# Optimization experiments

Measured on AMD Instinct MI355X. Metric: run time of the kernel, lower is better.

The kernel has to match this reference:

```python
import jax, jax.numpy as jnp
import numpy as np

# ---- static configuration (matches init_kwargs / input_specs) ----
B, N = 4, 128            # images, proposals per image
C = 256                  # feature channels (in_channels)
HF, WF = 23, 30          # feature map size (input 736x960 / 32)
PH, PW = 7, 7            # pooled_size
SCALE = 1.0 / 32.0       # scale_factor
HIMG, WIMG = HF * 32, WF * 32
KH = HF // PH + 2        # max rows any pooling bin can span
KW = WF // PW + 2        # max cols any pooling bin can span
HID, OUT = 256, 5
NEG = -1e30


def _roi_pool_one(f, box):
    """Quantized ROI max pooling for one proposal.
    f: (C, HF, WF) feature map; box: (4,) [x1,y1,x2,y2] in feature coords.
    Returns (C, PH, PW)."""
    box = jax.lax.stop_gradient(box)  # indices are non-differentiable
    x1 = jnp.clip(jnp.floor(box[0]).astype(jnp.int32), 0, WF - 1)
    y1 = jnp.clip(jnp.floor(box[1]).astype(jnp.int32), 0, HF - 1)
    roi_w = jnp.clip(jnp.ceil(box[2]).astype(jnp.int32) - x1, 1, WF)
    roi_h = jnp.clip(jnp.ceil(box[3]).astype(jnp.int32) - y1, 1, HF)
    ph = jnp.arange(PH)
    pw = jnp.arange(PW)
    hs = y1 + (ph * roi_h) // PH                       # bin row starts (PH,)
    he = y1 + ((ph + 1) * roi_h + PH - 1) // PH        # bin row ends (ceil)
    ws = x1 + (pw * roi_w) // PW
    we = x1 + ((pw + 1) * roi_w + PW - 1) // PW
    hidx = hs[:, None] + jnp.arange(KH)[None, :]       # (PH, KH)
    hval = (hidx < he[:, None]) & (hidx < HF)
    widx = ws[:, None] + jnp.arange(KW)[None, :]       # (PW, KW)
    wval = (widx < we[:, None]) & (widx < WF)
    rows = f[:, jnp.clip(hidx, 0, HF - 1), :]          # (C, PH, KH, WF) gather
    rmax = jnp.max(jnp.where(hval[None, :, :, None], rows, NEG), axis=2)  # (C, PH, WF)
    cols = rmax[:, :, jnp.clip(widx, 0, WF - 1)]       # (C, PH, PW, KW) gather
    return jnp.max(jnp.where(wval[None, None], cols, NEG), axis=3)        # (C, PH, PW)


# vmap over proposals, then over images: (B,C,HF,WF),(B,N,4) -> (B,N,C,PH,PW)
_roi_pool = jax.vmap(jax.vmap(_roi_pool_one, in_axes=(None, 0)), in_axes=(0, 0))


def setup_inputs() -> dict:
    key = jax.random.key(0)
    ks = jax.random.split(key, 8)
    features = jax.random.normal(ks[0], (B, C, HF, WF), jnp.float32)
    # valid proposals in image coordinates (min box side ~32 px)
    x1 = jax.random.uniform(ks[1], (B, N)) * (WIMG - 32.0)
    y1 = jax.random.uniform(ks[2], (B, N)) * (HIMG - 32.0)
    x2 = x1 + 32.0 + jax.random.uniform(ks[3], (B, N)) * (WIMG - 32.0 - x1)
    y2 = y1 + 32.0 + jax.random.uniform(ks[4], (B, N)) * (HIMG - 32.0 - y1)
    conf = jax.random.normal(ks[5], (B, N))
    proposals = jnp.stack([x1, y1, x2, y2, conf], axis=-1)  # (B, N, 5)
    W1 = jax.random.normal(ks[6], (HID, C * PH * PW), jnp.float32) * 0.01
    b1 = jnp.zeros((HID,), jnp.float32)
    W2 = jax.random.normal(ks[7], (OUT, HID), jnp.float32) * 0.01
    b2 = jnp.zeros((OUT,), jnp.float32)
    return {"features": features, "proposals": proposals,
            "W1": W1, "b1": b1, "W2": W2, "b2": b2}


def reference(features, proposals, W1, b1, W2, b2):
    boxes_feat = proposals[..., :4] * SCALE                 # image -> feature coords
    pooled = _roi_pool(features, boxes_feat)                # (B, N, C, PH, PW)
    flat = pooled.reshape(B, N, C * PH * PW)
    h = jax.nn.relu(jnp.einsum('bnf,hf->bnh', flat, W1) + b1)
    out = jnp.einsum('bnh,oh->bno', h, W2) + b2             # (B, N, 5)
    refined_boxes = proposals[..., :4] + out[..., :4]
    refined_conf = jax.nn.sigmoid(proposals[..., 4:5] + out[..., 4:5])
    return jnp.concatenate([refined_boxes, refined_conf], axis=-1)  # (B, N, 5)
```

## Files before the change

kernel.cpp:

```cpp
#include <hip/hip_runtime.h>
#include <math.h>

#define Bq 4
#define Nq 128
#define Cq 256
#define HFq 23
#define WFq 30
#define PHq 7
#define PWq 7
#define HIDq 256
#define OUTq 5
#define Fq (Cq*PHq*PWq)
#define Mq (Bq*Nq)
#define HWq (HFq*WFq)
#define SCALEq (1.0f/32.0f)
#define NEGq (-1e30f)
#define KHq 5
#define KWq 6
#define SPLITK 14
#define KCH (Fq/SPLITK)
#define BKq 64
#define KSTEPS (KCH/BKq)

typedef float f32x4 __attribute__((ext_vector_type(4)));
typedef __bf16 bf16x8 __attribute__((ext_vector_type(8)));
typedef unsigned short u16x8 __attribute__((ext_vector_type(8)));

__device__ __forceinline__ unsigned short f2b(float f) {
    unsigned int u = __float_as_uint(f);
    unsigned int r = (u + 0x7FFFu + ((u >> 16) & 1u)) >> 16;
    return (unsigned short)r;
}

__global__ __launch_bounds__(256) void k_prep(const float* __restrict__ feat,
                                              unsigned short* __restrict__ ft,
                                              const float* __restrict__ W1,
                                              unsigned short* __restrict__ w1p,
                                              float* __restrict__ h) {
    __shared__ __align__(16) unsigned short smem[Fq];
    int bid = blockIdx.x;
    int tid = threadIdx.x;
    if (bid < 704) {
        float (*t)[33] = (float (*)[33])smem;
        int bb  = bid / 176;
        int rem = bid % 176;
        int x0 = (rem % 22) * 32;
        int c0 = (rem / 22) * 32;
        int tx = tid & 31, ty = tid >> 5;
        const float* src = feat + (size_t)bb * Cq * HWq;
        unsigned short* dst = ft + (size_t)bb * HWq * Cq;
#pragma unroll
        for (int i = 0; i < 4; ++i) {
            int c = c0 + ty + i * 8;
            int x = x0 + tx;
            if (x < HWq) t[ty + i * 8][tx] = src[(size_t)c * HWq + x];
        }
        __syncthreads();
        int u = tid & 15, xl = tid >> 4;
#pragma unroll
        for (int i = 0; i < 2; ++i) {
            int xloc = xl + i * 16;
            int x = x0 + xloc;
            if (x < HWq) {
                ushort2 o;
                o.x = f2b(t[u * 2][xloc]);
                o.y = f2b(t[u * 2 + 1][xloc]);
                *(ushort2*)(dst + (size_t)x * Cq + c0 + u * 2) = o;
            }
        }
    } else if (bid < 960) {
        int j = bid - 704;
        const float4* src = (const float4*)(W1 + (size_t)j * Fq);
        for (int i = tid; i < Fq / 4; i += 256) {
            float4 v = src[i];
            ushort4 o;
            o.x = f2b(v.x); o.y = f2b(v.y); o.z = f2b(v.z); o.w = f2b(v.w);
            ((ushort4*)smem)[i] = o;
        }
        __syncthreads();
        uint4* dst = (uint4*)(w1p + (size_t)j * Fq);
        for (int i = tid; i < Fq / 8; i += 256) {
            int base = i * 8;
            int cell = base >> 8;
            int c0v = base & 255;
            unsigned short tmp[8];
#pragma unroll
            for (int u2 = 0; u2 < 8; ++u2) tmp[u2] = smem[(c0v + u2) * 49 + cell];
            dst[i] = *(const uint4*)tmp;
        }
    } else {
        f32x4* h4 = (f32x4*)h;
        int base = (bid - 960) * 4096;
        f32x4 z = {0.f, 0.f, 0.f, 0.f};
#pragma unroll
        for (int u2 = 0; u2 < 16; ++u2) h4[base + u2 * 256 + tid] = z;
    }
}

__global__ __launch_bounds__(256) void k_pool(const unsigned short* __restrict__ ft,
                                              const float* __restrict__ props,
                                              unsigned short* __restrict__ pooled) {
    int wave = threadIdx.x >> 6;
    int lane = threadIdx.x & 63;
    int half = lane >> 5;
    int cl = lane & 31;
    int g = blockIdx.y * 4 + wave;
    int m = blockIdx.x;
    int b = m >> 7;
    const float* pr = props + (size_t)m * 5;
    float b0 = pr[0] * SCALEq, b1v = pr[1] * SCALEq;
    float b2v = pr[2] * SCALEq, b3v = pr[3] * SCALEq;
    int x1 = min(max((int)floorf(b0), 0), WFq - 1);
    int y1 = min(max((int)floorf(b1v), 0), HFq - 1);
    int rw = min(max((int)ceilf(b2v) - x1, 1), WFq);
    int rh = min(max((int)ceilf(b3v) - y1, 1), HFq);
    const unsigned short* ftb = ft + (size_t)b * HWq * Cq + cl * 8;
    unsigned short* pm = pooled + (size_t)m * Fq + cl * 8;

    for (int cell = g; cell < PHq * PWq; cell += 8) {
        int ph = cell / 7;
        int pw = cell - ph * 7;
        int hs = y1 + (ph * rh) / PHq;
        int he = min(y1 + ((ph + 1) * rh + PHq - 1) / PHq, HFq);
        int ws = x1 + (pw * rw) / PWq;
        int we = min(x1 + ((pw + 1) * rw + PWq - 1) / PWq, WFq);
        float acc[8];
#pragma unroll
        for (int u = 0; u < 8; ++u) acc[u] = NEGq;
#pragma unroll
        for (int kh = 0; kh < KHq; ++kh) {
            if (hs + kh < he) {
                const unsigned short* rowp = ftb + (size_t)((hs + kh) * WFq) * Cq;
#pragma unroll
                for (int kw2 = 0; kw2 < 3; ++kw2) {
                    int w = ws + kw2 * 2 + half;
                    if (w < we) {
                        u16x8 v = *(const u16x8*)(rowp + (size_t)w * Cq);
#pragma unroll
                        for (int u = 0; u < 8; ++u)
                            acc[u] = fmaxf(acc[u], __uint_as_float((unsigned)v[u] << 16));
                    }
                }
            }
        }
#pragma unroll
        for (int u = 0; u < 8; ++u) acc[u] = fmaxf(acc[u], __shfl_xor(acc[u], 32));
        if (half == 0) {
            u16x8 o;
#pragma unroll
            for (int u = 0; u < 8; ++u) o[u] = f2b(acc[u]);
            *(u16x8*)(pm + (size_t)cell * Cq) = o;
        }
    }
}

__global__ __launch_bounds__(256) void k_gemm1(const unsigned short* __restrict__ pooled,
                                               const unsigned short* __restrict__ w1p,
                                               float* __restrict__ h) {
    __shared__ __align__(16) unsigned short As[2][64 * BKq];
    __shared__ __align__(16) unsigned short Bs[2][64 * BKq];
    int m0 = blockIdx.x * 64;
    int j0 = blockIdx.y * 64;
    int kz = blockIdx.z;
    int tid = threadIdx.x;
    int r = tid >> 2, qq = tid & 3;
    const uint4* ap = (const uint4*)(pooled + (size_t)(m0 + r) * Fq + (size_t)kz * KCH) + qq;
    const uint4* bp = (const uint4*)(w1p + (size_t)(j0 + r) * Fq + (size_t)kz * KCH) + qq;
    int lane = tid & 63, wv = tid >> 6;
    int q = lane >> 4, mr = lane & 15;
    f32x4 acc0 = {0.f, 0.f, 0.f, 0.f};
    f32x4 acc1 = {0.f, 0.f, 0.f, 0.f};
    f32x4 acc2 = {0.f, 0.f, 0.f, 0.f};
    f32x4 acc3 = {0.f, 0.f, 0.f, 0.f};
    int st1 = r * 8 + ((qq) ^ (r & 7));
    int st2 = r * 8 + ((qq ^ 4) ^ (r & 7));
    int sA = (wv * 16 + mr) * 8;
    int c0k0 = (q) ^ (mr & 7);
    int c0k1 = (q ^ 4) ^ (mr & 7);

    uint4 a0v = ap[0], a1v = ap[4];
    uint4 b0v = bp[0], b1v = bp[4];
    {
        uint4* aw = (uint4*)As[0];
        uint4* bw = (uint4*)Bs[0];
        aw[st1] = a0v; aw[st2] = a1v;
        bw[st1] = b0v; bw[st2] = b1v;
    }
    a0v = ap[8];  a1v = ap[12];
    b0v = bp[8];  b1v = bp[12];
    for (int s = 0; s < KSTEPS; ++s) {
        __syncthreads();
        int cur = s & 1;
        if (s + 1 < KSTEPS) {
            uint4* aw = (uint4*)As[cur ^ 1];
            uint4* bw = (uint4*)Bs[cur ^ 1];
            aw[st1] = a0v; aw[st2] = a1v;
            bw[st1] = b0v; bw[st2] = b1v;
            if (s + 2 < KSTEPS) {
                a0v = ap[(s + 2) * 8];     a1v = ap[(s + 2) * 8 + 4];
                b0v = bp[(s + 2) * 8];     b1v = bp[(s + 2) * 8 + 4];
            }
        }
        const bf16x8* Ab = (const bf16x8*)As[cur];
        const bf16x8* Bb = (const bf16x8*)Bs[cur];
        bf16x8 a0 = Ab[sA + c0k0];
        bf16x8 a1 = Ab[sA + c0k1];
        acc0 = __builtin_amdgcn_mfma_f32_16x16x32_bf16(a0, Bb[(0  + mr) * 8 + c0k0], acc0, 0, 0, 0);
        acc1 = __builtin_amdgcn_mfma_f32_16x16x32_bf16(a0, Bb[(16 + mr) * 8 + c0k0], acc1, 0, 0, 0);
        acc2 = __builtin_amdgcn_mfma_f32_16x16x32_bf16(a0, Bb[(32 + mr) * 8 + c0k0], acc2, 0, 0, 0);
        acc3 = __builtin_amdgcn_mfma_f32_16x16x32_bf16(a0, Bb[(48 + mr) * 8 + c0k0], acc3, 0, 0, 0);
        acc0 = __builtin_amdgcn_mfma_f32_16x16x32_bf16(a1, Bb[(0  + mr) * 8 + c0k1], acc0, 0, 0, 0);
        acc1 = __builtin_amdgcn_mfma_f32_16x16x32_bf16(a1, Bb[(16 + mr) * 8 + c0k1], acc1, 0, 0, 0);
        acc2 = __builtin_amdgcn_mfma_f32_16x16x32_bf16(a1, Bb[(32 + mr) * 8 + c0k1], acc2, 0, 0, 0);
        acc3 = __builtin_amdgcn_mfma_f32_16x16x32_bf16(a1, Bb[(48 + mr) * 8 + c0k1], acc3, 0, 0, 0);
    }
    int mb = m0 + wv * 16 + q * 4;
    int jj = j0 + mr;
#pragma unroll
    for (int r2 = 0; r2 < 4; ++r2) {
        float* row = h + (size_t)(mb + r2) * HIDq + jj;
        atomicAdd(row + 0,  acc0[r2]);
        atomicAdd(row + 16, acc1[r2]);
        atomicAdd(row + 32, acc2[r2]);
        atomicAdd(row + 48, acc3[r2]);
    }
}

__global__ __launch_bounds__(256) void k_tail(const float* __restrict__ h,
                                              const float* __restrict__ b1,
                                              const float* __restrict__ W2,
                                              const float* __restrict__ b2,
                                              const float* __restrict__ props,
                                              float* __restrict__ out) {
    __shared__ float red[OUTq][4];
    int m = blockIdx.x, j = threadIdx.x;
    float hv = fmaxf(h[(size_t)m * HIDq + j] + b1[j], 0.f);
    float p[OUTq];
#pragma unroll
    for (int o = 0; o < OUTq; ++o) p[o] = hv * W2[(size_t)o * HIDq + j];
    int lane = j & 63, wid = j >> 6;
#pragma unroll
    for (int o = 0; o < OUTq; ++o) {
        float v = p[o];
        v += __shfl_xor(v, 1);
        v += __shfl_xor(v, 2);
        v += __shfl_xor(v, 4);
        v += __shfl_xor(v, 8);
        v += __shfl_xor(v, 16);
        v += __shfl_xor(v, 32);
        if (lane == 0) red[o][wid] = v;
    }
    __syncthreads();
    if (j < OUTq) {
        float s = red[j][0] + red[j][1] + red[j][2] + red[j][3] + b2[j];
        float pv = props[(size_t)m * 5 + j];
        float r;
        if (j < 4) r = pv + s;
        else r = 1.f / (1.f + expf(-(pv + s)));
        out[(size_t)m * 5 + j] = r;
    }
}

extern "C" void kernel_launch(void* const* d_in, const int* in_sizes, int n_in,
                              void* d_out, int out_size, void* d_ws, size_t ws_size,
                              hipStream_t stream) {
    const float* feat  = (const float*)d_in[0];
    const float* props = (const float*)d_in[1];
    const float* W1    = (const float*)d_in[2];
    const float* b1    = (const float*)d_in[3];
    const float* W2    = (const float*)d_in[4];
    const float* b2    = (const float*)d_in[5];
    float* out = (float*)d_out;

    char* ws = (char*)d_ws;
    unsigned short* ft     = (unsigned short*)(ws);
    unsigned short* w1p    = (unsigned short*)(ws + 1413120);
    unsigned short* pooled = (unsigned short*)(ws + 7835648);
    float* h               = (float*)(ws + 20680704);

    k_prep<<<968, 256, 0, stream>>>(feat, ft, W1, w1p, h);
    k_pool<<<dim3(Mq, 2), 256, 0, stream>>>(ft, props, pooled);
    k_gemm1<<<dim3(8, 4, SPLITK), 256, 0, stream>>>(pooled, w1p, h);
    k_tail<<<Mq, 256, 0, stream>>>(h, b1, W2, b2, props, out);
}
```

Measured before the change: 119.7 us.

## Enlarge GEMM M-tile to 128, widen pooling grid, batch tail rows

The first GEMM now uses 128-row M tiles: each wave computes a 32x64 block, and every B fragment loaded from LDS feeds two MFMAs, so B reuse improves and the grid has half as many blocks. The pooling kernel launches four y-blocks instead of two, giving 16 waves per proposal with one cell stride each. The tail kernel handles 8 rows per block and reuses the b1 and W2 loads across them. The cost is more accumulator registers in the GEMM and fewer GEMM blocks to spread over the CUs.

```diff
diff --git a/kernel.cpp b/kernel.cpp
--- a/kernel.cpp
+++ b/kernel.cpp
@@ -20,6 +20,7 @@
 #define SPLITK 14
 #define KCH (Fq/SPLITK)
 #define BKq 64
+#define BMq 128
 #define KSTEPS (KCH/BKq)
 
 typedef float f32x4 __attribute__((ext_vector_type(4)));
@@ -117,7 +118,7 @@
     const unsigned short* ftb = ft + (size_t)b * HWq * Cq + cl * 8;
     unsigned short* pm = pooled + (size_t)m * Fq + cl * 8;
 
-    for (int cell = g; cell < PHq * PWq; cell += 8) {
+    for (int cell = g; cell < PHq * PWq; cell += 16) {
         int ph = cell / 7;
         int pw = cell - ph * 7;
         int hs = y1 + (ph * rh) / PHq;
@@ -157,72 +158,90 @@
 __global__ __launch_bounds__(256) void k_gemm1(const unsigned short* __restrict__ pooled,
                                                const unsigned short* __restrict__ w1p,
                                                float* __restrict__ h) {
-    __shared__ __align__(16) unsigned short As[2][64 * BKq];
+    __shared__ __align__(16) unsigned short As[2][BMq * BKq];
     __shared__ __align__(16) unsigned short Bs[2][64 * BKq];
-    int m0 = blockIdx.x * 64;
+    int m0 = blockIdx.x * BMq;
     int j0 = blockIdx.y * 64;
     int kz = blockIdx.z;
     int tid = threadIdx.x;
-    int r = tid >> 2, qq = tid & 3;
-    const uint4* ap = (const uint4*)(pooled + (size_t)(m0 + r) * Fq + (size_t)kz * KCH) + qq;
-    const uint4* bp = (const uint4*)(w1p + (size_t)(j0 + r) * Fq + (size_t)kz * KCH) + qq;
+    int rA = tid >> 1, cA = (tid & 1) * 4;
+    const uint4* ap = (const uint4*)(pooled + (size_t)(m0 + rA) * Fq + (size_t)kz * KCH) + cA;
+    int rB = tid >> 2, qq = tid & 3;
+    const uint4* bp = (const uint4*)(w1p + (size_t)(j0 + rB) * Fq + (size_t)kz * KCH) + qq;
     int lane = tid & 63, wv = tid >> 6;
     int q = lane >> 4, mr = lane & 15;
-    f32x4 acc0 = {0.f, 0.f, 0.f, 0.f};
-    f32x4 acc1 = {0.f, 0.f, 0.f, 0.f};
-    f32x4 acc2 = {0.f, 0.f, 0.f, 0.f};
-    f32x4 acc3 = {0.f, 0.f, 0.f, 0.f};
-    int st1 = r * 8 + ((qq) ^ (r & 7));
-    int st2 = r * 8 + ((qq ^ 4) ^ (r & 7));
-    int sA = (wv * 16 + mr) * 8;
-    int c0k0 = (q) ^ (mr & 7);
-    int c0k1 = (q ^ 4) ^ (mr & 7);
-
-    uint4 a0v = ap[0], a1v = ap[4];
-    uint4 b0v = bp[0], b1v = bp[4];
+    f32x4 acc00 = {0.f,0.f,0.f,0.f}, acc01 = {0.f,0.f,0.f,0.f};
+    f32x4 acc02 = {0.f,0.f,0.f,0.f}, acc03 = {0.f,0.f,0.f,0.f};
+    f32x4 acc10 = {0.f,0.f,0.f,0.f}, acc11 = {0.f,0.f,0.f,0.f};
+    f32x4 acc12 = {0.f,0.f,0.f,0.f}, acc13 = {0.f,0.f,0.f,0.f};
+    int swA = rA & 7, swB = rB & 7;
+    int stB1 = rB * 8 + (qq ^ swB);
+    int stB2 = rB * 8 + ((qq ^ 4) ^ swB);
+
+    uint4 av[4], bv0, bv1;
+#pragma unroll
+    for (int u = 0; u < 4; ++u) av[u] = ap[u];
+    bv0 = bp[0]; bv1 = bp[4];
     {
         uint4* aw = (uint4*)As[0];
         uint4* bw = (uint4*)Bs[0];
-        aw[st1] = a0v; aw[st2] = a1v;
-        bw[st1] = b0v; bw[st2] = b1v;
-    }
-    a0v = ap[8];  a1v = ap[12];
-    b0v = bp[8];  b1v = bp[12];
+#pragma unroll
+        for (int u = 0; u < 4; ++u) aw[rA * 8 + ((cA + u) ^ swA)] = av[u];
+        bw[stB1] = bv0; bw[stB2] = bv1;
+    }
+#pragma unroll
+    for (int u = 0; u < 4; ++u) av[u] = ap[8 + u];
+    bv0 = bp[8]; bv1 = bp[12];
+
     for (int s = 0; s < KSTEPS; ++s) {
         __syncthreads();
         int cur = s & 1;
         if (s + 1 < KSTEPS) {
             uint4* aw = (uint4*)As[cur ^ 1];
             uint4* bw = (uint4*)Bs[cur ^ 1];
-            aw[st1] = a0v; aw[st2] = a1v;
-            bw[st1] = b0v; bw[st2] = b1v;
+#pragma unroll
+            for (int u = 0; u < 4; ++u) aw[rA * 8 + ((cA + u) ^ swA)] = av[u];
+            bw[stB1] = bv0; bw[stB2] = bv1;
             if (s + 2 < KSTEPS) {
-                a0v = ap[(s + 2) * 8];     a1v = ap[(s + 2) * 8 + 4];
-                b0v = bp[(s + 2) * 8];     b1v = bp[(s + 2) * 8 + 4];
+#pragma unroll
+                for (int u = 0; u < 4; ++u) av[u] = ap[(s + 2) * 8 + u];
+                bv0 = bp[(s + 2) * 8]; bv1 = bp[(s + 2) * 8 + 4];
             }
         }
         const bf16x8* Ab = (const bf16x8*)As[cur];
         const bf16x8* Bb = (const bf16x8*)Bs[cur];
-        bf16x8 a0 = Ab[sA + c0k0];
-        bf16x8 a1 = Ab[sA + c0k1];
-        acc0 = __builtin_amdgcn_mfma_f32_16x16x32_bf16(a0, Bb[(0  + mr) * 8 + c0k0], acc0, 0, 0, 0);
-        acc1 = __builtin_amdgcn_mfma_f32_16x16x32_bf16(a0, Bb[(16 + mr) * 8 + c0k0], acc1, 0, 0, 0);
-        acc2 = __builtin_amdgcn_mfma_f32_16x16x32_bf16(a0, Bb[(32 + mr) * 8 + c0k0], acc2, 0, 0, 0);
-        acc3 = __builtin_amdgcn_mfma_f32_16x16x32_bf16(a0, Bb[(48 + mr) * 8 + c0k0], acc3, 0, 0, 0);
-        acc0 = __builtin_amdgcn_mfma_f32_16x16x32_bf16(a1, Bb[(0  + mr) * 8 + c0k1], acc0, 0, 0, 0);
-        acc1 = __builtin_amdgcn_mfma_f32_16x16x32_bf16(a1, Bb[(16 + mr) * 8 + c0k1], acc1, 0, 0, 0);
-        acc2 = __builtin_amdgcn_mfma_f32_16x16x32_bf16(a1, Bb[(32 + mr) * 8 + c0k1], acc2, 0, 0, 0);
-        acc3 = __builtin_amdgcn_mfma_f32_16x16x32_bf16(a1, Bb[(48 + mr) * 8 + c0k1], acc3, 0, 0, 0);
-    }
-    int mb = m0 + wv * 16 + q * 4;
+#pragma unroll
+        for (int kk = 0; kk < 2; ++kk) {
+            int ck = (kk * 4 + q) ^ (mr & 7);
+            bf16x8 a0 = Ab[(wv * 32 + mr) * 8 + ck];
+            bf16x8 a1 = Ab[(wv * 32 + 16 + mr) * 8 + ck];
+            bf16x8 bb0 = Bb[(0  + mr) * 8 + ck];
+            bf16x8 bb1 = Bb[(16 + mr) * 8 + ck];
+            bf16x8 bb2 = Bb[(32 + mr) * 8 + ck];
+            bf16x8 bb3 = Bb[(48 + mr) * 8 + ck];
+            acc00 = __builtin_amdgcn_mfma_f32_16x16x32_bf16(a0, bb0, acc00, 0, 0, 0);
+            acc01 = __builtin_amdgcn_mfma_f32_16x16x32_bf16(a0, bb1, acc01, 0, 0, 0);
+            acc02 = __builtin_amdgcn_mfma_f32_16x16x32_bf16(a0, bb2, acc02, 0, 0, 0);
+            acc03 = __builtin_amdgcn_mfma_f32_16x16x32_bf16(a0, bb3, acc03, 0, 0, 0);
+            acc10 = __builtin_amdgcn_mfma_f32_16x16x32_bf16(a1, bb0, acc10, 0, 0, 0);
+            acc11 = __builtin_amdgcn_mfma_f32_16x16x32_bf16(a1, bb1, acc11, 0, 0, 0);
+            acc12 = __builtin_amdgcn_mfma_f32_16x16x32_bf16(a1, bb2, acc12, 0, 0, 0);
+            acc13 = __builtin_amdgcn_mfma_f32_16x16x32_bf16(a1, bb3, acc13, 0, 0, 0);
+        }
+    }
     int jj = j0 + mr;
 #pragma unroll
     for (int r2 = 0; r2 < 4; ++r2) {
-        float* row = h + (size_t)(mb + r2) * HIDq + jj;
-        atomicAdd(row + 0,  acc0[r2]);
-        atomicAdd(row + 16, acc1[r2]);
-        atomicAdd(row + 32, acc2[r2]);
-        atomicAdd(row + 48, acc3[r2]);
+        float* row0 = h + (size_t)(m0 + wv * 32 + q * 4 + r2) * HIDq + jj;
+        atomicAdd(row0 + 0,  acc00[r2]);
+        atomicAdd(row0 + 16, acc01[r2]);
+        atomicAdd(row0 + 32, acc02[r2]);
+        atomicAdd(row0 + 48, acc03[r2]);
+        float* row1 = h + (size_t)(m0 + wv * 32 + 16 + q * 4 + r2) * HIDq + jj;
+        atomicAdd(row1 + 0,  acc10[r2]);
+        atomicAdd(row1 + 16, acc11[r2]);
+        atomicAdd(row1 + 32, acc12[r2]);
+        atomicAdd(row1 + 48, acc13[r2]);
     }
 }
 
@@ -232,32 +251,42 @@
                                               const float* __restrict__ b2,
                                               const float* __restrict__ props,
                                               float* __restrict__ out) {
-    __shared__ float red[OUTq][4];
-    int m = blockIdx.x, j = threadIdx.x;
-    float hv = fmaxf(h[(size_t)m * HIDq + j] + b1[j], 0.f);
-    float p[OUTq];
-#pragma unroll
-    for (int o = 0; o < OUTq; ++o) p[o] = hv * W2[(size_t)o * HIDq + j];
+    __shared__ float red[8][OUTq][4];
+    int j = threadIdx.x;
     int lane = j & 63, wid = j >> 6;
-#pragma unroll
-    for (int o = 0; o < OUTq; ++o) {
-        float v = p[o];
-        v += __shfl_xor(v, 1);
-        v += __shfl_xor(v, 2);
-        v += __shfl_xor(v, 4);
-        v += __shfl_xor(v, 8);
-        v += __shfl_xor(v, 16);
-        v += __shfl_xor(v, 32);
-        if (lane == 0) red[o][wid] = v;
+    int m0 = blockIdx.x * 8;
+    float b1v = b1[j];
+    float hv[8];
+#pragma unroll
+    for (int i = 0; i < 8; ++i)
+        hv[i] = fmaxf(h[(size_t)(m0 + i) * HIDq + j] + b1v, 0.f);
+    float w2v[OUTq];
+#pragma unroll
+    for (int o = 0; o < OUTq; ++o) w2v[o] = W2[(size_t)o * HIDq + j];
+#pragma unroll
+    for (int i = 0; i < 8; ++i) {
+#pragma unroll
+        for (int o = 0; o < OUTq; ++o) {
+            float v = hv[i] * w2v[o];
+            v += __shfl_xor(v, 1);
+            v += __shfl_xor(v, 2);
+            v += __shfl_xor(v, 4);
+            v += __shfl_xor(v, 8);
+            v += __shfl_xor(v, 16);
+            v += __shfl_xor(v, 32);
+            if (lane == 0) red[i][o][wid] = v;
+        }
     }
     __syncthreads();
-    if (j < OUTq) {
-        float s = red[j][0] + red[j][1] + red[j][2] + red[j][3] + b2[j];
-        float pv = props[(size_t)m * 5 + j];
+    if (j < 8 * OUTq) {
+        int i = j / OUTq, o = j - i * OUTq;
+        int m = m0 + i;
+        float s = red[i][o][0] + red[i][o][1] + red[i][o][2] + red[i][o][3] + b2[o];
+        float pv = props[(size_t)m * 5 + o];
         float r;
-        if (j < 4) r = pv + s;
+        if (o < 4) r = pv + s;
         else r = 1.f / (1.f + expf(-(pv + s)));
-        out[(size_t)m * 5 + j] = r;
+        out[(size_t)m * 5 + o] = r;
     }
 }
 
@@ -279,7 +308,7 @@
     float* h               = (float*)(ws + 20680704);
 
     k_prep<<<968, 256, 0, stream>>>(feat, ft, W1, w1p, h);
-    k_pool<<<dim3(Mq, 2), 256, 0, stream>>>(ft, props, pooled);
-    k_gemm1<<<dim3(8, 4, SPLITK), 256, 0, stream>>>(pooled, w1p, h);
-    k_tail<<<Mq, 256, 0, stream>>>(h, b1, W2, b2, props, out);
-}
+    k_pool<<<dim3(Mq, 4), 256, 0, stream>>>(ft, props, pooled);
+    k_gemm1<<<dim3(Mq / BMq, HIDq / 64, SPLITK), 256, 0, stream>>>(pooled, w1p, h);
+    k_tail<<<Mq / 8, 256, 0, stream>>>(h, b1, W2, b2, props, out);
+}
```

Result: slower. 131.3 us (+9.7%).
